# Optimization experiments

Measured on AMD Instinct MI355X. Metric: run time of the kernel, lower is better.

Reference implementation:

```python
import jax, jax.numpy as jnp
import numpy as np

KERNEL_NUM = 21
SIGMA = 0.1
EXACT_SIGMA = 0.001

def _kernel_params(k=KERNEL_NUM, sigma=SIGMA, exact_sigma=EXACT_SIGMA):
    step = 1.0 / (k - 1)
    left = -1.0 + step
    right = 1.0 - step
    mu = np.hstack([np.arange(left, right, (right - left) / (k - 2)), right, 1.0])
    sig = np.where(mu == 1.0, exact_sigma, sigma)
    return jnp.asarray(mu, jnp.float32), jnp.asarray(sig, jnp.float32)

MU, SIG = _kernel_params()

def setup_inputs() -> dict:
    key = jax.random.key(0)
    ks = jax.random.split(key, 11)
    B, LQ, LD, V, E = 1024, 20, 200, 100000, 128
    return {
        "q1": jax.random.randint(ks[0], (B, LQ), 0, V),
        "d1": jax.random.randint(ks[1], (B, LD), 0, V),
        "q2": jax.random.randint(ks[2], (B, LQ), 0, V),
        "d2": jax.random.randint(ks[3], (B, LD), 0, V),
        "emb": jax.random.normal(ks[4], (V, E), jnp.float32),
        "W1": jax.random.normal(ks[5], (10, 21), jnp.float32) * 0.1,
        "b1": jax.random.normal(ks[6], (10,), jnp.float32) * 0.1,
        "W2": jax.random.normal(ks[7], (5, 10), jnp.float32) * 0.1,
        "b2": jax.random.normal(ks[8], (5,), jnp.float32) * 0.1,
        "W3": jax.random.normal(ks[9], (1, 5), jnp.float32) * 0.1,
        "b3": jax.random.normal(ks[10], (1,), jnp.float32) * 0.1,
    }

def _matching_matrix(emb, q_ids, d_ids, alpha=1e-6):
    q = emb[q_ids]  # [B,LQ,E]
    d = emb[d_ids]  # [B,LD,E]
    nom = jnp.einsum('bqe,bde->bqd', q, d)
    qn = jnp.sqrt(jnp.sum(q * q, axis=2) + alpha)  # [B,LQ]
    dn = jnp.sqrt(jnp.sum(d * d, axis=2) + alpha)  # [B,LD]
    return nom / (qn[:, :, None] * dn[:, None, :])  # [B,LQ,LD]

def _apply_kernels(M):
    # M: [B,LQ,LD] -> phi: [B,LQ,LD,K]
    phi = jnp.exp(-jnp.square(M[..., None] - MU) / (2.0 * SIG * SIG))
    return jnp.sum(jnp.log1p(jnp.sum(phi, axis=2)), axis=1)  # [B,K]

def _mlp(x, W1, b1, W2, b2, W3, b3):
    x = jax.nn.relu(x)
    x = x @ W1.T + b1
    x = jax.nn.relu(x)
    x = x @ W2.T + b2
    x = jax.nn.relu(x)
    return x @ W3.T + b3  # [B,1]

def _predict(emb, q, d, W1, b1, W2, b2, W3, b3):
    M = _matching_matrix(emb, q, d)
    k = _apply_kernels(M)
    return _mlp(k, W1, b1, W2, b2, W3, b3)

def reference(q1, d1, q2, d2, emb, W1, b1, W2, b2, W3, b3):
    l1 = _predict(emb, q1, d1, W1, b1, W2, b2, W3, b3)
    l2 = _predict(emb, q2, d2, W1, b1, W2, b2, W3, b3)
    return jax.nn.sigmoid(l1 - l2)  # [B,1]
```

## Files before the change

kernel.cpp:

```cpp
#include <hip/hip_runtime.h>

#define NB 1024
#define LQ 20
#define LD 200
#define E4 32
#define NK 21
#define NTILE 13

typedef __attribute__((ext_vector_type(8))) short bf16x8;
typedef __attribute__((ext_vector_type(4))) float f32x4;

__device__ __forceinline__ short f2bf(float f, float& back) {
    unsigned u = __builtin_bit_cast(unsigned, f);
    unsigned r = (u + 0x7FFFu + ((u >> 16) & 1u)) >> 16;
    back = __builtin_bit_cast(float, r << 16);
    return (short)r;
}

__device__ __forceinline__ bf16x8 make_frag(float4 f0, float4 f1, float& sq) {
    bf16x8 v; float bk;
    v[0] = f2bf(f0.x, bk); sq += bk * bk;
    v[1] = f2bf(f0.y, bk); sq += bk * bk;
    v[2] = f2bf(f0.z, bk); sq += bk * bk;
    v[3] = f2bf(f0.w, bk); sq += bk * bk;
    v[4] = f2bf(f1.x, bk); sq += bk * bk;
    v[5] = f2bf(f1.y, bk); sq += bk * bk;
    v[6] = f2bf(f1.z, bk); sq += bk * bk;
    v[7] = f2bf(f1.w, bk); sq += bk * bk;
    return v;
}

__device__ __forceinline__ float fast_exp2(float x) {
#if __has_builtin(__builtin_amdgcn_exp2f)
    return __builtin_amdgcn_exp2f(x);
#else
    return __expf(x * 0.69314718056f);
#endif
}

__device__ __forceinline__ void rbf_accum(float m, float* S) {
    const float x = m - 0.05f;
    const float p = fast_exp2(-72.13475204f * x * x);
    S[10] += p;
    float u = fast_exp2(fmaf(m, 14.4269504089f, -1.44269504089f));
    float q = p;
    #pragma unroll
    for (int k = 11; k <= 19; ++k) {
        q *= u;
        S[k] += q;
        u *= 0.36787944117f;
    }
    float v = fast_exp2(m * -14.4269504089f);
    q = p;
    #pragma unroll
    for (int k = 9; k >= 0; --k) {
        q *= v;
        S[k] += q;
        v *= 0.36787944117f;
    }
    const float d = m - 1.0f;
    S[20] += fast_exp2(-721347.5204f * d * d);
}

__global__ __launch_bounds__(256, 3) void knrm_main(
    const int* __restrict__ q1, const int* __restrict__ d1,
    const int* __restrict__ q2, const int* __restrict__ d2,
    const float* __restrict__ emb,
    const float* __restrict__ W1, const float* __restrict__ b1,
    const float* __restrict__ W2, const float* __restrict__ b2,
    const float* __restrict__ W3, const float* __restrict__ b3,
    float* __restrict__ logits)
{
    __shared__ float sPhiW[4][LQ][NK];
    __shared__ float sX[NK];
    __shared__ float sH1[10];
    __shared__ float sH2[5];

    const int bp   = blockIdx.x;
    const int b    = bp & (NB - 1);
    const int pred = bp >> 10;
    const int t    = threadIdx.x;
    const int lane = t & 63, wave = t >> 6;
    const int c    = lane & 15, quad = lane >> 4;
    const int* __restrict__ qi = pred ? q2 : q1;
    const int* __restrict__ di = pred ? d2 : d1;
    const float4* emb4 = (const float4*)emb;

    int qid[2];
    #pragma unroll
    for (int Mt = 0; Mt < 2; ++Mt) {
        int row = Mt * 16 + c; row = row < LQ ? row : LQ - 1;
        qid[Mt] = qi[b * LQ + row];
    }
    int idv[4];
    #pragma unroll
    for (int tt = 0; tt < 4; ++tt) {
        int j = (wave + tt * 4) * 16 + c; j = j < LD ? j : LD - 1;
        idv[tt] = di[b * LD + j];
    }

    bf16x8 aF[2][4];
    float rqA = 0.f, rqB = 0.f;
    #pragma unroll
    for (int Mt = 0; Mt < 2; ++Mt) {
        const float4* qb = emb4 + (size_t)(unsigned)qid[Mt] * E4;
        float qs = 0.f;
        #pragma unroll
        for (int ks = 0; ks < 4; ++ks) {
            float4 f0 = qb[ks * 8 + quad * 2];
            float4 f1 = qb[ks * 8 + quad * 2 + 1];
            aF[Mt][ks] = make_frag(f0, f1, qs);
        }
        if (Mt == 1 && c >= LQ - 16) {
            #pragma unroll
            for (int ks = 0; ks < 4; ++ks) aF[Mt][ks] = (bf16x8)0;
            qs = 0.f;
        }
        qs += __shfl_xor(qs, 16);
        qs += __shfl_xor(qs, 32);
        const float rq = rsqrtf(qs + 1e-6f);
        if (Mt == 0) rqA = rq; else rqB = rq;
    }

    float S0[NK], S1[NK];
    #pragma unroll
    for (int k = 0; k < NK; ++k) { S0[k] = 0.f; S1[k] = 0.f; }

    #pragma unroll
    for (int tt = 0; tt < 4; ++tt) {
        const int tile = wave + tt * 4;
        if (tile >= NTILE) break;

        const float4* db = emb4 + (size_t)(unsigned)idv[tt] * E4;
        bf16x8 bF[4];
        float dsq = 0.f;
        #pragma unroll
        for (int ks = 0; ks < 4; ++ks) {
            float4 f0 = db[ks * 8 + quad * 2];
            float4 f1 = db[ks * 8 + quad * 2 + 1];
            bF[ks] = make_frag(f0, f1, dsq);
        }
        if (tile * 16 + c >= LD) {
            #pragma unroll
            for (int ks = 0; ks < 4; ++ks) bF[ks] = (bf16x8)0;
            dsq = 0.f;
        }
        dsq += __shfl_xor(dsq, 16);
        dsq += __shfl_xor(dsq, 32);
        const float rdc = rsqrtf(dsq + 1e-6f);
        float rdv[4];
        #pragma unroll
        for (int r = 0; r < 4; ++r) rdv[r] = __shfl(rdc, quad * 4 + r);

        f32x4 acc0 = {0.f, 0.f, 0.f, 0.f};
        f32x4 acc1 = {0.f, 0.f, 0.f, 0.f};
        #pragma unroll
        for (int ks = 0; ks < 4; ++ks) {
            acc0 = __builtin_amdgcn_mfma_f32_16x16x32_bf16(bF[ks], aF[0][ks], acc0, 0, 0, 0);
            acc1 = __builtin_amdgcn_mfma_f32_16x16x32_bf16(bF[ks], aF[1][ks], acc1, 0, 0, 0);
        }

        #pragma unroll
        for (int r = 0; r < 4; ++r)
            rbf_accum(acc0[r] * rdv[r] * rqA, S0);

        float m1[4];
        #pragma unroll
        for (int r = 0; r < 4; ++r) m1[r] = acc1[r] * rdv[r] * rqB;
        const int src = (lane & 48) | ((lane >> 2) & 3);
        const float g0 = __shfl(m1[0], src);
        const float g1 = __shfl(m1[1], src);
        const float g2 = __shfl(m1[2], src);
        const float g3 = __shfl(m1[3], src);
        const int rsel = lane & 3;
        const float mv = (rsel == 0) ? g0 : (rsel == 1) ? g1 : (rsel == 2) ? g2 : g3;
        rbf_accum(mv, S1);
    }

    #pragma unroll
    for (int k = 0; k < NK; ++k) {
        S0[k] += __shfl_xor(S0[k], 16);
        S0[k] += __shfl_xor(S0[k], 32);
        S1[k] += __shfl_xor(S1[k], 1);
        S1[k] += __shfl_xor(S1[k], 2);
        S1[k] += __shfl_xor(S1[k], 16);
        S1[k] += __shfl_xor(S1[k], 32);
    }
    if (quad == 0) {
        #pragma unroll
        for (int k = 0; k < NK; ++k) sPhiW[wave][c][k] = S0[k];
    }
    if ((lane & 51) == 0) {
        #pragma unroll
        for (int k = 0; k < NK; ++k) sPhiW[wave][16 + (lane >> 2)][k] = S1[k];
    }
    __syncthreads();

    if (t < NK) {
        const float mu_t = 0.1f * (float)t - 0.95f;
        const float pad  = (t < 20) ? 8.0f * fast_exp2(-72.13475204f * mu_t * mu_t) : 0.0f;
        float s = 0.f;
        #pragma unroll
        for (int i = 0; i < LQ; ++i) {
            const float v = sPhiW[0][i][t] + sPhiW[1][i][t]
                          + sPhiW[2][i][t] + sPhiW[3][i][t] - pad;
            s += __logf(1.0f + v);
        }
        sX[t] = fmaxf(s, 0.f);
    }
    __syncthreads();

    if (t < 10) {
        float v = b1[t];
        #pragma unroll
        for (int k = 0; k < NK; ++k) v += W1[t * NK + k] * sX[k];
        sH1[t] = fmaxf(v, 0.f);
    }
    __syncthreads();

    if (t < 5) {
        float v = b2[t];
        #pragma unroll
        for (int k = 0; k < 10; ++k) v += W2[t * 10 + k] * sH1[k];
        sH2[t] = fmaxf(v, 0.f);
    }
    __syncthreads();

    if (t == 0) {
        float v = b3[0];
        #pragma unroll
        for (int k = 0; k < 5; ++k) v += W3[k] * sH2[k];
        logits[pred * NB + b] = v;
    }
}

__global__ void knrm_combine(const float* __restrict__ logits, float* __restrict__ out)
{
    const int b = blockIdx.x * blockDim.x + threadIdx.x;
    if (b < NB) {
        out[b] = 1.0f / (1.0f + __expf(logits[NB + b] - logits[b]));
    }
}

extern "C" void kernel_launch(void* const* d_in, const int* in_sizes, int n_in,
                              void* d_out, int out_size, void* d_ws, size_t ws_size,
                              hipStream_t stream) {
    float* logits = (float*)d_ws;
    knrm_main<<<2 * NB, 256, 0, stream>>>(
        (const int*)d_in[0], (const int*)d_in[1],
        (const int*)d_in[2], (const int*)d_in[3],
        (const float*)d_in[4],
        (const float*)d_in[5], (const float*)d_in[6],
        (const float*)d_in[7], (const float*)d_in[8],
        (const float*)d_in[9], (const float*)d_in[10],
        logits);
    knrm_combine<<<(NB + 255) / 256, 256, 0, stream>>>(logits, (float*)d_out);
}
```

Baseline: 148.3 us.

## Fuse both predictions into one block and drop the combine kernel

Each block now handles both query/doc pairs for a batch element, with two waves per prediction covering up to 7 doc tiles each, and computes the sigmoid difference directly, so the separate combine launch and the logits workspace round trip go away. The bf16 conversion uses the packed float2-to-bfloat162 intrinsic instead of manual rounding, and launch bounds ask for 4 blocks per SM. Each wave now does more serial tile work with longer register lifetimes (idv[7]), which may increase register pressure. There are also half as many blocks, which may reduce latency hiding.

```diff
diff --git a/kernel.cpp b/kernel.cpp
--- a/kernel.cpp
+++ b/kernel.cpp
@@ -1,4 +1,5 @@
 #include <hip/hip_runtime.h>
+#include <hip/hip_bf16.h>
 
 #define NB 1024
 #define LQ 20
@@ -10,24 +11,27 @@
 typedef __attribute__((ext_vector_type(8))) short bf16x8;
 typedef __attribute__((ext_vector_type(4))) float f32x4;
 
-__device__ __forceinline__ short f2bf(float f, float& back) {
-    unsigned u = __builtin_bit_cast(unsigned, f);
-    unsigned r = (u + 0x7FFFu + ((u >> 16) & 1u)) >> 16;
-    back = __builtin_bit_cast(float, r << 16);
-    return (short)r;
-}
+__device__ __forceinline__ unsigned cvt2(float lo, float hi) {
+    __hip_bfloat162 h = __float22bfloat162_rn(make_float2(lo, hi));
+    unsigned u;
+    __builtin_memcpy(&u, &h, 4);
+    return u;
+}
+__device__ __forceinline__ float lo2f(unsigned p) { return __builtin_bit_cast(float, p << 16); }
+__device__ __forceinline__ float hi2f(unsigned p) { return __builtin_bit_cast(float, p & 0xFFFF0000u); }
 
 __device__ __forceinline__ bf16x8 make_frag(float4 f0, float4 f1, float& sq) {
-    bf16x8 v; float bk;
-    v[0] = f2bf(f0.x, bk); sq += bk * bk;
-    v[1] = f2bf(f0.y, bk); sq += bk * bk;
-    v[2] = f2bf(f0.z, bk); sq += bk * bk;
-    v[3] = f2bf(f0.w, bk); sq += bk * bk;
-    v[4] = f2bf(f1.x, bk); sq += bk * bk;
-    v[5] = f2bf(f1.y, bk); sq += bk * bk;
-    v[6] = f2bf(f1.z, bk); sq += bk * bk;
-    v[7] = f2bf(f1.w, bk); sq += bk * bk;
-    return v;
+    union { unsigned u[4]; bf16x8 v; } r;
+    r.u[0] = cvt2(f0.x, f0.y);
+    r.u[1] = cvt2(f0.z, f0.w);
+    r.u[2] = cvt2(f1.x, f1.y);
+    r.u[3] = cvt2(f1.z, f1.w);
+    #pragma unroll
+    for (int i = 0; i < 4; ++i) {
+        const float a = lo2f(r.u[i]); sq = fmaf(a, a, sq);
+        const float b = hi2f(r.u[i]); sq = fmaf(b, b, sq);
+    }
+    return r.v;
 }
 
 __device__ __forceinline__ float fast_exp2(float x) {
@@ -62,25 +66,24 @@
     S[20] += fast_exp2(-721347.5204f * d * d);
 }
 
-__global__ __launch_bounds__(256, 3) void knrm_main(
+__global__ __launch_bounds__(256, 4) void knrm_main(
     const int* __restrict__ q1, const int* __restrict__ d1,
     const int* __restrict__ q2, const int* __restrict__ d2,
     const float* __restrict__ emb,
     const float* __restrict__ W1, const float* __restrict__ b1,
     const float* __restrict__ W2, const float* __restrict__ b2,
     const float* __restrict__ W3, const float* __restrict__ b3,
-    float* __restrict__ logits)
+    float* __restrict__ out)
 {
     __shared__ float sPhiW[4][LQ][NK];
-    __shared__ float sX[NK];
-    __shared__ float sH1[10];
-    __shared__ float sH2[5];
-
-    const int bp   = blockIdx.x;
-    const int b    = bp & (NB - 1);
-    const int pred = bp >> 10;
+    __shared__ float sX[2][NK];
+    __shared__ float sH1[2][10];
+    __shared__ float sH2[2][5];
+
+    const int b    = blockIdx.x;
     const int t    = threadIdx.x;
     const int lane = t & 63, wave = t >> 6;
+    const int pred = wave >> 1, wv = wave & 1;
     const int c    = lane & 15, quad = lane >> 4;
     const int* __restrict__ qi = pred ? q2 : q1;
     const int* __restrict__ di = pred ? d2 : d1;
@@ -92,11 +95,12 @@
         int row = Mt * 16 + c; row = row < LQ ? row : LQ - 1;
         qid[Mt] = qi[b * LQ + row];
     }
-    int idv[4];
-    #pragma unroll
-    for (int tt = 0; tt < 4; ++tt) {
-        int j = (wave + tt * 4) * 16 + c; j = j < LD ? j : LD - 1;
-        idv[tt] = di[b * LD + j];
+    int idv[7];
+    #pragma unroll
+    for (int tt = 0; tt < 7; ++tt) {
+        const int tile = wv + 2 * tt;
+        int j = tile * 16 + c; j = j < LD ? j : LD - 1;
+        idv[tt] = (tile < NTILE) ? di[b * LD + j] : 0;
     }
 
     bf16x8 aF[2][4];
@@ -127,8 +131,8 @@
     for (int k = 0; k < NK; ++k) { S0[k] = 0.f; S1[k] = 0.f; }
 
     #pragma unroll
-    for (int tt = 0; tt < 4; ++tt) {
-        const int tile = wave + tt * 4;
+    for (int tt = 0; tt < 7; ++tt) {
+        const int tile = wv + 2 * tt;
         if (tile >= NTILE) break;
 
         const float4* db = emb4 + (size_t)(unsigned)idv[tt] * E4;
@@ -196,63 +200,57 @@
     }
     __syncthreads();
 
-    if (t < NK) {
-        const float mu_t = 0.1f * (float)t - 0.95f;
-        const float pad  = (t < 20) ? 8.0f * fast_exp2(-72.13475204f * mu_t * mu_t) : 0.0f;
+    const int ew = t >> 6, et = t & 63;
+
+    if (ew < 2 && et < NK) {
+        const float mu_t = 0.1f * (float)et - 0.95f;
+        const float pad  = (et < 20) ? 8.0f * fast_exp2(-72.13475204f * mu_t * mu_t) : 0.0f;
         float s = 0.f;
         #pragma unroll
         for (int i = 0; i < LQ; ++i) {
-            const float v = sPhiW[0][i][t] + sPhiW[1][i][t]
-                          + sPhiW[2][i][t] + sPhiW[3][i][t] - pad;
+            const float v = sPhiW[2 * ew][i][et] + sPhiW[2 * ew + 1][i][et] - pad;
             s += __logf(1.0f + v);
         }
-        sX[t] = fmaxf(s, 0.f);
-    }
-    __syncthreads();
-
-    if (t < 10) {
-        float v = b1[t];
-        #pragma unroll
-        for (int k = 0; k < NK; ++k) v += W1[t * NK + k] * sX[k];
-        sH1[t] = fmaxf(v, 0.f);
-    }
-    __syncthreads();
-
-    if (t < 5) {
-        float v = b2[t];
-        #pragma unroll
-        for (int k = 0; k < 10; ++k) v += W2[t * 10 + k] * sH1[k];
-        sH2[t] = fmaxf(v, 0.f);
+        sX[ew][et] = fmaxf(s, 0.f);
+    }
+    __syncthreads();
+
+    if (ew < 2 && et < 10) {
+        float v = b1[et];
+        #pragma unroll
+        for (int k = 0; k < NK; ++k) v += W1[et * NK + k] * sX[ew][k];
+        sH1[ew][et] = fmaxf(v, 0.f);
+    }
+    __syncthreads();
+
+    if (ew < 2 && et < 5) {
+        float v = b2[et];
+        #pragma unroll
+        for (int k = 0; k < 10; ++k) v += W2[et * 10 + k] * sH1[ew][k];
+        sH2[ew][et] = fmaxf(v, 0.f);
     }
     __syncthreads();
 
     if (t == 0) {
-        float v = b3[0];
-        #pragma unroll
-        for (int k = 0; k < 5; ++k) v += W3[k] * sH2[k];
-        logits[pred * NB + b] = v;
-    }
-}
-
-__global__ void knrm_combine(const float* __restrict__ logits, float* __restrict__ out)
-{
-    const int b = blockIdx.x * blockDim.x + threadIdx.x;
-    if (b < NB) {
-        out[b] = 1.0f / (1.0f + __expf(logits[NB + b] - logits[b]));
+        float l0 = b3[0], l1 = b3[0];
+        #pragma unroll
+        for (int k = 0; k < 5; ++k) {
+            l0 += W3[k] * sH2[0][k];
+            l1 += W3[k] * sH2[1][k];
+        }
+        out[b] = 1.0f / (1.0f + __expf(l1 - l0));
     }
 }
 
 extern "C" void kernel_launch(void* const* d_in, const int* in_sizes, int n_in,
                               void* d_out, int out_size, void* d_ws, size_t ws_size,
                               hipStream_t stream) {
-    float* logits = (float*)d_ws;
-    knrm_main<<<2 * NB, 256, 0, stream>>>(
+    knrm_main<<<NB, 256, 0, stream>>>(
         (const int*)d_in[0], (const int*)d_in[1],
         (const int*)d_in[2], (const int*)d_in[3],
         (const float*)d_in[4],
         (const float*)d_in[5], (const float*)d_in[6],
         (const float*)d_in[7], (const float*)d_in[8],
         (const float*)d_in[9], (const float*)d_in[10],
-        logits);
-    knrm_combine<<<(NB + 255) / 256, 256, 0, stream>>>(logits, (float*)d_out);
-}
+        (float*)d_out);
+}
```

Result: slower. 217.3 us (+46.5%).
